# Kernel tuning notes

Measured on AMD Instinct MI355X. Metric: run time of the kernel, lower is better.

The kernel has to match this reference:

```python
import jax, jax.numpy as jnp
import numpy as np

B, C, H, W, NA = 2, 512, 25, 25, 9
A = H * W * NA  # 5625 anchors
PROB_T = 0.5
OVL_T = 0.5


def _make_anchors():
    ys, xs = np.meshgrid(np.arange(H), np.arange(W), indexing='ij')
    cx = (xs + 0.5) / W
    cy = (ys + 0.5) / H
    boxes = []
    for s in (0.1, 0.2, 0.4):
        for r in (0.5, 1.0, 2.0):
            w = s * np.sqrt(r)
            h = s / np.sqrt(r)
            boxes.append(np.stack([cx - w / 2, cy - h / 2, cx + w / 2, cy + h / 2], -1))
    anc = np.stack(boxes, axis=2)  # [H, W, 9, 4] matches [B,H,W,9*4] reshape order
    return jnp.asarray(anc.reshape(-1, 4), jnp.float32)


def setup_inputs() -> dict:
    key = jax.random.key(0)
    ks = jax.random.split(key, 4)
    x = jax.random.normal(ks[0], (B, C, H, W), jnp.float32)
    conv_w = jax.random.normal(ks[1], (512, 512, 3, 3), jnp.float32) * (1.0 / np.sqrt(512 * 9))
    conv_b = jnp.zeros((512,), jnp.float32)
    reg_w = jax.random.normal(ks[2], (36, 512), jnp.float32) * 0.02
    reg_b = jnp.zeros((36,), jnp.float32)
    cls_w = jax.random.normal(ks[3], (9, 512), jnp.float32) * 0.05
    cls_b = jnp.zeros((9,), jnp.float32)
    anchors = _make_anchors()
    return {"x": x, "conv_w": conv_w, "conv_b": conv_b, "reg_w": reg_w,
            "reg_b": reg_b, "cls_w": cls_w, "cls_b": cls_b, "anchors": anchors}


def reference(x, conv_w, conv_b, reg_w, reg_b, cls_w, cls_b, anchors):
    # --- RPN forward ---
    h = jax.lax.conv_general_dilated(x, conv_w, (1, 1), 'SAME',
                                     dimension_numbers=('NCHW', 'OIHW', 'NCHW'))
    h = jax.nn.relu(h + conv_b[None, :, None, None])
    box = jnp.einsum('bchw,oc->bhwo', h, reg_w) + reg_b  # [B,H,W,36] (== permute NHWC)
    cls = jnp.einsum('bchw,oc->bhwo', h, cls_w) + cls_b  # [B,H,W,9]
    offsets = box.reshape(B, A, 4)
    logits = cls.reshape(B, A)
    # --- detect: sigmoid + threshold ---
    probs = jax.nn.sigmoid(logits)
    valid = probs > PROB_T
    # --- box decode: gcxgcy -> cxcy -> xy (SSD-style, anchors given in xy) ---
    a_cx = (anchors[:, 0] + anchors[:, 2]) * 0.5
    a_cy = (anchors[:, 1] + anchors[:, 3]) * 0.5
    a_w = anchors[:, 2] - anchors[:, 0]
    a_h = anchors[:, 3] - anchors[:, 1]
    cx = offsets[..., 0] * a_w / 10.0 + a_cx
    cy = offsets[..., 1] * a_h / 10.0 + a_cy
    bw = jnp.exp(offsets[..., 2] / 5.0) * a_w
    bh = jnp.exp(offsets[..., 3] / 5.0) * a_h
    boxes = jnp.stack([cx - bw / 2, cy - bh / 2, cx + bw / 2, cy + bh / 2], -1)  # [B,A,4]
    # --- sort descending by score; invalid anchors sorted last and pre-suppressed ---
    sort_key = jnp.where(valid, probs, -1.0)
    order = jnp.argsort(-sort_key, axis=-1)
    sb = jnp.take_along_axis(boxes, order[..., None], axis=1)  # sorted boxes
    ss = jnp.take_along_axis(probs, order, axis=1)             # sorted scores
    sv = jnp.take_along_axis(valid, order, axis=1)             # sorted validity

    def per_image(b, v):
        x1, y1, x2, y2 = b[:, 0], b[:, 1], b[:, 2], b[:, 3]
        area = (x2 - x1) * (y2 - y1)
        iw = jnp.clip(jnp.minimum(x2[:, None], x2[None, :]) - jnp.maximum(x1[:, None], x1[None, :]), 0.0)
        ih = jnp.clip(jnp.minimum(y2[:, None], y2[None, :]) - jnp.maximum(y1[:, None], y1[None, :]), 0.0)
        inter = iw * ih
        ov = inter / (area[:, None] + area[None, :] - inter)  # [A,A] Jaccard
        sup0 = (~v).astype(jnp.int32)  # invalid anchors never considered

        def body(i, sup):
            cand = jnp.maximum(sup, (ov[i] > OVL_T).astype(jnp.int32)).at[i].set(0)
            return jnp.where(sup[i] > 0, sup, cand)  # skip if already suppressed

        sup = jax.lax.fori_loop(0, A, body, sup0)
        return (1 - sup) * v.astype(jnp.int32)

    keep = jax.vmap(per_image)(sb, sv)  # [B,A] 1 = kept detection
    return jnp.concatenate([sb, ss[..., None], keep[..., None].astype(jnp.float32)], -1)  # [B,A,6]
```

## Files before the change

### kernel.cpp

```cpp
#include <hip/hip_runtime.h>
#include <cstdint>
#include <cstddef>

#define AA 5625
#define MROWS 5760

__global__ __launch_bounds__(256) void k_wt(const float* __restrict__ cw,
                                            float* __restrict__ wt,
                                            int* __restrict__ Vcnt) {
  if (blockIdx.x == 0 && threadIdx.x < 2) Vcnt[threadIdx.x] = 0;
  __shared__ float t[64][65];
  int kb = (blockIdx.x % 72) * 64;
  int ob = (blockIdx.x / 72) * 64;
  int col = threadIdx.x & 63;
  int rr  = threadIdx.x >> 6;
#pragma unroll
  for (int it = 0; it < 16; ++it) {
    int row = rr + it * 4;
    t[row][col] = cw[(size_t)(ob + row) * 4608 + kb + col];
  }
  __syncthreads();
#pragma unroll
  for (int it = 0; it < 16; ++it) {
    int row = rr + it * 4;
    wt[(size_t)(kb + row) * 512 + ob + col] = t[col][row];
  }
}

__global__ void k_xpad(const float* __restrict__ x, float* __restrict__ xp) {
  int n = blockIdx.x * 256 + threadIdx.x;
  if (n >= 884736) return;
  int c = n & 31;
  int r = (n >> 5) % 27;
  int rest = (n >> 5) / 27;
  float v = 0.f;
  int oy = r - 1, ox = c - 1;
  if (oy >= 0 && oy < 25 && ox >= 0 && ox < 25)
    v = x[(size_t)rest * 625 + oy * 25 + ox];
  xp[n] = v;
}

__global__ __launch_bounds__(256) void k_conv(const float* __restrict__ wt,
                                              const float* __restrict__ xp,
                                              double* __restrict__ hpart,
                                              int Kper) {
  int cpx = gridDim.x >> 3;
  int flat = blockIdx.x;
  int logical = (flat & 7) * cpx + (flat >> 3);
  int sharer = logical % 10;
  int s      = logical / 10;
  int Nt = s & 7;
  int ks = s >> 3;
  int b  = sharer / 5;
  int Mt = sharer % 5;

  int tid = threadIdx.x;
  int m0  = Mt * 128;
  int oc0 = Nt * 64;
  int R  = (tid >> 6) * 32 + ((tid >> 4) & 3) * 8;
  int cb = 2 * (tid & 15);

  __shared__ __align__(16) float As[2][18][128];
  __shared__ __align__(16) float Bs[2][18][64];

  double acc[8][4];
#pragma unroll
  for (int i = 0; i < 8; ++i)
#pragma unroll
    for (int j = 0; j < 4; ++j) acc[i][j] = 0.0;

  int kbase = ks * Kper;
  int nchunk = Kper / 18;

  int ldsoA[9], aoff[9];
#pragma unroll
  for (int t = 0; t < 9; ++t) {
    int s2 = tid + 256 * t;
    int row = s2 >> 7, col = s2 & 127;
    ldsoA[t] = row * 128 + col;
    int m = m0 + col;
    bool av = (m < 625);
    int mm = av ? m : 0;
    int icl = (row >= 9) ? 1 : 0;
    int tap = row - 9 * icl;
    int dy = tap / 3, dx = tap - 3 * dy;
    int yy = mm / 25, xx = mm - yy * 25;
    int ao = (icl * 27 + yy + dy) * 32 + xx + dx;
    aoff[t] = av ? ao : -1;
  }
  int ldsoB[5], boffB[5];
  bool bval[5];
#pragma unroll
  for (int t = 0; t < 5; ++t) {
    int s2 = tid + 256 * t;
    bval[t] = (s2 < 1152);
    int s2c = bval[t] ? s2 : 0;
    int row = s2c >> 6, col = s2c & 63;
    ldsoB[t] = row * 64 + col;
    boffB[t] = row * 512 + oc0 + col;
  }
  const float* wbase = wt + (size_t)kbase * 512;
  const float* abase = xp + (size_t)(b * 512 + kbase / 9) * 864;

  float rA[9], rB[5];

#define LOADCH(CH) {                                                          \
    int k0e = (CH) * (18 * 512);                                              \
    int a0e = (CH) * (2 * 864);                                               \
    _Pragma("unroll")                                                         \
    for (int t = 0; t < 9; ++t)                                               \
      rA[t] = (aoff[t] >= 0) ? abase[a0e + aoff[t]] : 0.f;                    \
    _Pragma("unroll")                                                         \
    for (int t = 0; t < 5; ++t)                                               \
      rB[t] = bval[t] ? wbase[k0e + boffB[t]] : 0.f;                          \
  }
#define WRITECH(BUF) {                                                        \
    _Pragma("unroll")                                                         \
    for (int t = 0; t < 9; ++t)                                               \
      ((float*)As[BUF])[ldsoA[t]] = rA[t];                                    \
    _Pragma("unroll")                                                         \
    for (int t = 0; t < 5; ++t)                                               \
      if (bval[t]) ((float*)Bs[BUF])[ldsoB[t]] = rB[t];                       \
  }

  LOADCH(0);
  WRITECH(0);
  __syncthreads();

  for (int ch = 0; ch < nchunk; ++ch) {
    int cur = ch & 1, nxt = cur ^ 1;
    int chn = (ch + 1 < nchunk) ? (ch + 1) : (nchunk - 1);
    LOADCH(chn);
#pragma unroll 2
    for (int kk = 0; kk < 18; ++kk) {
      float4 a0 = *(const float4*)&As[cur][kk][R];
      float4 a1 = *(const float4*)&As[cur][kk][R + 4];
      float2 b0 = *(const float2*)&Bs[cur][kk][cb];
      float2 b1 = *(const float2*)&Bs[cur][kk][cb + 32];
      double ad[8] = {(double)a0.x, (double)a0.y, (double)a0.z, (double)a0.w,
                      (double)a1.x, (double)a1.y, (double)a1.z, (double)a1.w};
      double bd[4] = {(double)b0.x, (double)b0.y, (double)b1.x, (double)b1.y};
#pragma unroll
      for (int i = 0; i < 8; ++i)
#pragma unroll
        for (int j = 0; j < 4; ++j) acc[i][j] += ad[i] * bd[j];
    }
    if (ch + 1 < nchunk) {
      __syncthreads();
      WRITECH(nxt);
      __syncthreads();
    }
  }

  double* hb = hpart + ((size_t)(ks * 2 + b) * 625) * 512 + oc0 + cb;
#pragma unroll
  for (int i = 0; i < 8; ++i) {
    int mm = m0 + R + i;
    if (mm < 625) {
      double* p = hb + (size_t)mm * 512;
      double2 v0; v0.x = acc[i][0]; v0.y = acc[i][1];
      double2 v1; v1.x = acc[i][2]; v1.y = acc[i][3];
      *(double2*)p        = v0;
      *(double2*)(p + 32) = v1;
    }
  }
#undef LOADCH
#undef WRITECH
}

__device__ __forceinline__ double shfl_down_d(double x, int off) {
  long long v = __double_as_longlong(x);
  int lo = __shfl_down((int)(unsigned int)(v & 0xffffffffLL), off);
  int hi = __shfl_down((int)(v >> 32), off);
  return __longlong_as_double(((long long)hi << 32) | (unsigned int)lo);
}

__global__ __launch_bounds__(256) void k_heads(
    const double* __restrict__ hpart, const float* __restrict__ conv_b,
    const float* __restrict__ reg_w, const float* __restrict__ reg_b,
    const float* __restrict__ cls_w, const float* __restrict__ cls_b,
    const float* __restrict__ anchors, float* __restrict__ boxesraw,
    float* __restrict__ probs, unsigned long long* __restrict__ keys,
    unsigned int* __restrict__ rank, int nsplit) {
  int pos = blockIdx.x % 625;
  int b   = blockIdx.x / 625;
  int tid = threadIdx.x;
  __shared__ double hv[512];
  __shared__ double res[45];
  for (int c = tid; c < 512; c += 256) {
    double s = 0.0;
    for (int k = 0; k < nsplit; ++k)
      s += hpart[(((size_t)k * 2 + b) * 625 + pos) * 512 + c];
    s += (double)conv_b[c];
    hv[c] = s > 0.0 ? s : 0.0;
  }
  __syncthreads();
  int wv = tid >> 6, l = tid & 63;
  for (int o = wv; o < 45; o += 4) {
    const float* wrow = (o < 36) ? (reg_w + (size_t)o * 512)
                                 : (cls_w + (size_t)(o - 36) * 512);
    double s = 0.0;
#pragma unroll
    for (int kk = 0; kk < 8; ++kk)
      s += hv[l + kk * 64] * (double)wrow[l + kk * 64];
#pragma unroll
    for (int d = 32; d > 0; d >>= 1) s += shfl_down_d(s, d);
    if (l == 0) res[o] = s + (double)((o < 36) ? reg_b[o] : cls_b[o - 36]);
  }
  __syncthreads();
  if (tid < 9) {
    int na = tid;
    int a = pos * 9 + na;
    double o0 = res[na * 4 + 0], o1 = res[na * 4 + 1];
    double o2 = res[na * 4 + 2], o3 = res[na * 4 + 3];
    double logit = res[36 + na];
    float4 anc = *(const float4*)(anchors + (size_t)a * 4);
    double a_cx = ((double)anc.x + (double)anc.z) * 0.5;
    double a_cy = ((double)anc.y + (double)anc.w) * 0.5;
    double a_w = (double)anc.z - (double)anc.x;
    double a_h = (double)anc.w - (double)anc.y;
    double cx = o0 * a_w / 10.0 + a_cx;
    double cy = o1 * a_h / 10.0 + a_cy;
    double bw = exp(o2 / 5.0) * a_w;
    double bh = exp(o3 / 5.0) * a_h;
    float4 box = make_float4((float)(cx - bw / 2.0), (float)(cy - bh / 2.0),
                             (float)(cx + bw / 2.0), (float)(cy + bh / 2.0));
    size_t ga = (size_t)b * AA + a;
    *(float4*)(boxesraw + ga * 4) = box;
    float p = (float)(1.0 / (1.0 + exp(-logit)));
    probs[ga] = p;
    bool valid = p > 0.5f;
    float f = -(valid ? p : -1.0f);
    unsigned int u = __float_as_uint(f);
    u = (u & 0x80000000u) ? ~u : (u | 0x80000000u);
    keys[ga] = (((unsigned long long)u) << 32) | (unsigned int)a;
    rank[ga] = 0u;
  }
}

__global__ __launch_bounds__(256) void k_count(
    const unsigned long long* __restrict__ keys, unsigned int* __restrict__ rank) {
  int b = blockIdx.z;
  int i = blockIdx.x * 256 + threadIdx.x;
  __shared__ unsigned long long sj[1024];
  unsigned long long my = (i < AA) ? keys[(size_t)b * AA + i] : 0ULL;
  int j0 = blockIdx.y * 1024;
  for (int jj = threadIdx.x; jj < 1024; jj += 256) {
    int j = j0 + jj;
    sj[jj] = (j < AA) ? keys[(size_t)b * AA + j] : ~0ULL;
  }
  __syncthreads();
  int cnt = 0;
#pragma unroll 8
  for (int jj = 0; jj < 1024; ++jj) cnt += (sj[jj] < my) ? 1 : 0;
  if (i < AA && cnt) atomicAdd(&rank[(size_t)b * AA + i], (unsigned)cnt);
}

__global__ void k_perm(const unsigned long long* __restrict__ keys,
                       const unsigned int* __restrict__ rank,
                       unsigned int* __restrict__ perm, int* __restrict__ Vcnt) {
  int idx = blockIdx.x * 256 + threadIdx.x;
  if (idx >= 2 * AA) return;
  int b = idx / AA, i = idx - b * AA;
  unsigned long long k = keys[idx];
  unsigned int r = rank[idx];
  perm[(size_t)b * AA + r] = (unsigned)i;
  if (!(k >> 63)) atomicAdd(&Vcnt[b], 1);
}

__global__ void k_assembly(const unsigned int* __restrict__ perm,
                           const float* __restrict__ boxesraw,
                           const float* __restrict__ probs,
                           float* __restrict__ out, float4* __restrict__ sb4) {
  int idx = blockIdx.x * 256 + threadIdx.x;
  if (idx >= 2 * AA) return;
  int b = idx / AA;
  unsigned int pa = perm[idx];
  float4 bx = *(const float4*)(boxesraw + ((size_t)b * AA + pa) * 4);
  float p = probs[(size_t)b * AA + pa];
  float* o = out + (size_t)idx * 6;
  o[0] = bx.x; o[1] = bx.y; o[2] = bx.z; o[3] = bx.w; o[4] = p; o[5] = 0.f;
  sb4[idx] = bx;
}

__global__ __launch_bounds__(256) void k_maskT(const float4* __restrict__ sb4,
                                               const int* __restrict__ Vcnt,
                                               ulonglong2* __restrict__ maskT) {
  int b = blockIdx.y;
  int V = Vcnt[b];
  int i = blockIdx.x * 4 + (threadIdx.x >> 6);
  if (i >= V) return;
  int lane = threadIdx.x & 63;
  float4 bif = sb4[(size_t)b * AA + i];
  double bix = bif.x, biy = bif.y, biz = bif.z, biw = bif.w;
  double ai = (biz - bix) * (biw - biy);
  unsigned long long lo = 0, hi = 0;
#pragma unroll 4
  for (int w = 0; w < 88; ++w) {
    int j = w * 64 + lane;
    int jc = (j < AA) ? j : (AA - 1);
    float4 c = sb4[(size_t)b * AA + jc];
    double aj = ((double)c.z - (double)c.x) * ((double)c.w - (double)c.y);
    double iw = fmin(biz, (double)c.z) - fmax(bix, (double)c.x);
    double ih = fmin(biw, (double)c.w) - fmax(biy, (double)c.y);
    iw = iw > 0.0 ? iw : 0.0;
    ih = ih > 0.0 ? ih : 0.0;
    double inter = iw * ih;
    bool bit = (inter + inter > ai + aj - inter) && (j != i) && (j < AA);
    unsigned long long bb = bit ? 1ULL : 0ULL;
    if (w < 64) lo |= bb << w;
    else        hi |= bb << (w - 64);
  }
  ulonglong2 v; v.x = lo; v.y = hi;
  maskT[((size_t)b * MROWS + i) * 64 + lane] = v;
}

#define NMS_STEP(Q, J)                                                        \
  {                                                                           \
    int i = base + (J);                                                       \
    if (i < V) {                                                              \
      int w = i >> 6, t = i & 63;                                             \
      if (t == 0) {                                                           \
        unsigned long long cbit = (w < 64) ? (colLo >> w) : (colHi >> (w - 64)); \
        supw = __ballot((int)(cbit & 1ULL));                                  \
      }                                                                       \
      if (!((supw >> t) & 1ULL)) {                                            \
        colLo |= Q.x; colHi |= Q.y;                                           \
        unsigned long long cbit = (w < 64) ? (colLo >> w) : (colHi >> (w - 64)); \
        supw = __ballot((int)(cbit & 1ULL));                                  \
        if (lane == 0) out[((size_t)b * AA + i) * 6 + 5] = 1.0f;              \
      }                                                                       \
    }                                                                         \
    Q = mt[(size_t)(i + 16) * 64 + lane];                                     \
  }

__global__ __launch_bounds__(64) void k_nms(const ulonglong2* __restrict__ maskT,
                                            const int* __restrict__ Vcnt,
                                            float* __restrict__ out) {
  int b = blockIdx.x;
  int lane = threadIdx.x;
  int V = Vcnt[b];
  const ulonglong2* mt = maskT + (size_t)b * MROWS * 64;
  unsigned long long colLo = 0, colHi = 0, supw = 0;
  ulonglong2 q00 = mt[(size_t)0  * 64 + lane], q01 = mt[(size_t)1  * 64 + lane];
  ulonglong2 q02 = mt[(size_t)2  * 64 + lane], q03 = mt[(size_t)3  * 64 + lane];
  ulonglong2 q04 = mt[(size_t)4  * 64 + lane], q05 = mt[(size_t)5  * 64 + lane];
  ulonglong2 q06 = mt[(size_t)6  * 64 + lane], q07 = mt[(size_t)7  * 64 + lane];
  ulonglong2 q08 = mt[(size_t)8  * 64 + lane], q09 = mt[(size_t)9  * 64 + lane];
  ulonglong2 q10 = mt[(size_t)10 * 64 + lane], q11 = mt[(size_t)11 * 64 + lane];
  ulonglong2 q12 = mt[(size_t)12 * 64 + lane], q13 = mt[(size_t)13 * 64 + lane];
  ulonglong2 q14 = mt[(size_t)14 * 64 + lane], q15 = mt[(size_t)15 * 64 + lane];
  for (int base = 0; base < V; base += 16) {
    NMS_STEP(q00, 0)  NMS_STEP(q01, 1)  NMS_STEP(q02, 2)  NMS_STEP(q03, 3)
    NMS_STEP(q04, 4)  NMS_STEP(q05, 5)  NMS_STEP(q06, 6)  NMS_STEP(q07, 7)
    NMS_STEP(q08, 8)  NMS_STEP(q09, 9)  NMS_STEP(q10, 10) NMS_STEP(q11, 11)
    NMS_STEP(q12, 12) NMS_STEP(q13, 13) NMS_STEP(q14, 14) NMS_STEP(q15, 15)
  }
}
#undef NMS_STEP

extern "C" void kernel_launch(void* const* d_in, const int* in_sizes, int n_in,
                              void* d_out, int out_size, void* d_ws, size_t ws_size,
                              hipStream_t stream) {
  const float* x      = (const float*)d_in[0];
  const float* conv_w = (const float*)d_in[1];
  const float* conv_b = (const float*)d_in[2];
  const float* reg_w  = (const float*)d_in[3];
  const float* reg_b  = (const float*)d_in[4];
  const float* cls_w  = (const float*)d_in[5];
  const float* cls_b  = (const float*)d_in[6];
  const float* anchors= (const float*)d_in[7];
  float* out = (float*)d_out;
  char* ws = (char*)d_ws;

  size_t off = 0;
  auto alloc = [&](size_t bytes) {
    size_t o = off;
    off += (bytes + 255) & ~(size_t)255;
    return o;
  };
  size_t o_wt   = alloc(4608ULL * 512 * 4);
  size_t o_xp   = alloc(884736ULL * 4);
  size_t o_box  = alloc(2ULL * AA * 4 * 4);
  size_t o_prob = alloc(2ULL * AA * 4);
  size_t o_keys = alloc(2ULL * AA * 8);
  size_t o_rank = alloc(2ULL * AA * 4);
  size_t o_perm = alloc(2ULL * AA * 4);
  size_t o_sb4  = alloc(2ULL * AA * 16);
  size_t o_V    = alloc(256);
  size_t o_maskT= alloc(2ULL * MROWS * 64 * 16);
  size_t fixed = off;

  int nsplit = 1;
  const int cands[5] = {16, 8, 4, 2, 1};
  for (int ci = 0; ci < 5; ++ci) {
    size_t need = fixed + (size_t)cands[ci] * 2 * 625 * 512 * 8;
    if (need <= ws_size) { nsplit = cands[ci]; break; }
  }
  size_t o_hp = alloc((size_t)nsplit * 2 * 625 * 512 * 8);

  float* wtp   = (float*)(ws + o_wt);
  float* xpp   = (float*)(ws + o_xp);
  float* boxp  = (float*)(ws + o_box);
  float* probp = (float*)(ws + o_prob);
  unsigned long long* keysp = (unsigned long long*)(ws + o_keys);
  unsigned int* rankp = (unsigned int*)(ws + o_rank);
  unsigned int* permp = (unsigned int*)(ws + o_perm);
  float4* sb4p = (float4*)(ws + o_sb4);
  int* Vp      = (int*)(ws + o_V);
  ulonglong2* maskTp = (ulonglong2*)(ws + o_maskT);
  double* hpp  = (double*)(ws + o_hp);

  k_wt<<<dim3(576), dim3(256), 0, stream>>>(conv_w, wtp, Vp);
  k_xpad<<<dim3(3456), dim3(256), 0, stream>>>(x, xpp);
  k_conv<<<dim3(80 * nsplit), dim3(256), 0, stream>>>(wtp, xpp, hpp, 4608 / nsplit);
  k_heads<<<dim3(1250), dim3(256), 0, stream>>>(hpp, conv_b, reg_w, reg_b,
                                                cls_w, cls_b, anchors, boxp,
                                                probp, keysp, rankp, nsplit);
  k_count<<<dim3(22, 6, 2), dim3(256), 0, stream>>>(keysp, rankp);
  k_perm<<<dim3(44), dim3(256), 0, stream>>>(keysp, rankp, permp, Vp);
  k_assembly<<<dim3(44), dim3(256), 0, stream>>>(permp, boxp, probp, out, sb4p);
  k_maskT<<<dim3(1407, 2), dim3(256), 0, stream>>>(sb4p, Vp, maskTp);
  k_nms<<<dim3(2), dim3(64), 0, stream>>>(maskTp, Vp, out);
}
```

Baseline: 531.6 us.

## Widen conv tile to 128x128 with fp64 LDS staging and unroll split-K reduce

The conv GEMM tile grows from 128x64 to 128x128 output channels per block, so each thread computes an 8x8 fp64 accumulator block. The grid is halved to match. Operands are now converted to double once when written into shared memory, so the inner loop no longer converts each float it reads, and the k-chunk shrinks from 18 to 9 to keep LDS size fixed. The heads kernel also unrolls the split-K partial sum for nsplit=16 so all 16 loads are issued at once. The trade-offs are much higher register pressure (64 fp64 accumulators), fewer blocks, and more LDS bandwidth per element.

After: 698.8 us. 1.31x slower.

```diff
diff --git a/kernel.cpp b/kernel.cpp
--- a/kernel.cpp
+++ b/kernel.cpp
@@ -49,78 +49,71 @@
   int logical = (flat & 7) * cpx + (flat >> 3);
   int sharer = logical % 10;
   int s      = logical / 10;
-  int Nt = s & 7;
-  int ks = s >> 3;
+  int Nt = s & 3;
+  int ks = s >> 2;
   int b  = sharer / 5;
   int Mt = sharer % 5;
 
   int tid = threadIdx.x;
   int m0  = Mt * 128;
-  int oc0 = Nt * 64;
+  int oc0 = Nt * 128;
   int R  = (tid >> 6) * 32 + ((tid >> 4) & 3) * 8;
   int cb = 2 * (tid & 15);
 
-  __shared__ __align__(16) float As[2][18][128];
-  __shared__ __align__(16) float Bs[2][18][64];
-
-  double acc[8][4];
+  __shared__ __align__(16) double As[2][9][128];
+  __shared__ __align__(16) double Bs[2][9][128];
+
+  double acc[8][8];
 #pragma unroll
   for (int i = 0; i < 8; ++i)
 #pragma unroll
-    for (int j = 0; j < 4; ++j) acc[i][j] = 0.0;
+    for (int j = 0; j < 8; ++j) acc[i][j] = 0.0;
 
   int kbase = ks * Kper;
-  int nchunk = Kper / 18;
-
-  int ldsoA[9], aoff[9];
-#pragma unroll
-  for (int t = 0; t < 9; ++t) {
+  int nchunk = Kper / 9;
+
+  int ldso[5], aoff[5], boff[5];
+  bool v4 = (tid < 128);
+#pragma unroll
+  for (int t = 0; t < 5; ++t) {
     int s2 = tid + 256 * t;
+    if (s2 >= 1152) s2 = 0;
     int row = s2 >> 7, col = s2 & 127;
-    ldsoA[t] = row * 128 + col;
+    ldso[t] = row * 128 + col;
+    boff[t] = row * 512 + oc0 + col;
     int m = m0 + col;
     bool av = (m < 625);
     int mm = av ? m : 0;
-    int icl = (row >= 9) ? 1 : 0;
-    int tap = row - 9 * icl;
-    int dy = tap / 3, dx = tap - 3 * dy;
+    int dy = row / 3, dx = row - 3 * dy;
     int yy = mm / 25, xx = mm - yy * 25;
-    int ao = (icl * 27 + yy + dy) * 32 + xx + dx;
-    aoff[t] = av ? ao : -1;
-  }
-  int ldsoB[5], boffB[5];
-  bool bval[5];
-#pragma unroll
-  for (int t = 0; t < 5; ++t) {
-    int s2 = tid + 256 * t;
-    bval[t] = (s2 < 1152);
-    int s2c = bval[t] ? s2 : 0;
-    int row = s2c >> 6, col = s2c & 63;
-    ldsoB[t] = row * 64 + col;
-    boffB[t] = row * 512 + oc0 + col;
+    aoff[t] = av ? ((yy + dy) * 32 + xx + dx) : -1;
   }
   const float* wbase = wt + (size_t)kbase * 512;
   const float* abase = xp + (size_t)(b * 512 + kbase / 9) * 864;
 
-  float rA[9], rB[5];
+  float rA[5], rB[5];
 
 #define LOADCH(CH) {                                                          \
-    int k0e = (CH) * (18 * 512);                                              \
-    int a0e = (CH) * (2 * 864);                                               \
+    int k0e = (CH) * (9 * 512);                                               \
+    int a0e = (CH) * 864;                                                     \
     _Pragma("unroll")                                                         \
-    for (int t = 0; t < 9; ++t)                                               \
+    for (int t = 0; t < 4; ++t) {                                             \
       rA[t] = (aoff[t] >= 0) ? abase[a0e + aoff[t]] : 0.f;                    \
-    _Pragma("unroll")                                                         \
-    for (int t = 0; t < 5; ++t)                                               \
-      rB[t] = bval[t] ? wbase[k0e + boffB[t]] : 0.f;                          \
+      rB[t] = wbase[k0e + boff[t]];                                           \
+    }                                                                         \
+    rA[4] = (v4 && aoff[4] >= 0) ? abase[a0e + aoff[4]] : 0.f;                \
+    rB[4] = v4 ? wbase[k0e + boff[4]] : 0.f;                                  \
   }
 #define WRITECH(BUF) {                                                        \
     _Pragma("unroll")                                                         \
-    for (int t = 0; t < 9; ++t)                                               \
-      ((float*)As[BUF])[ldsoA[t]] = rA[t];                                    \
-    _Pragma("unroll")                                                         \
-    for (int t = 0; t < 5; ++t)                                               \
-      if (bval[t]) ((float*)Bs[BUF])[ldsoB[t]] = rB[t];                       \
+    for (int t = 0; t < 4; ++t) {                                             \
+      ((double*)As[BUF])[ldso[t]] = (double)rA[t];                            \
+      ((double*)Bs[BUF])[ldso[t]] = (double)rB[t];                            \
+    }                                                                         \
+    if (v4) {                                                                 \
+      ((double*)As[BUF])[ldso[4]] = (double)rA[4];                            \
+      ((double*)Bs[BUF])[ldso[4]] = (double)rB[4];                            \
+    }                                                                         \
   }
 
   LOADCH(0);
@@ -131,19 +124,22 @@
     int cur = ch & 1, nxt = cur ^ 1;
     int chn = (ch + 1 < nchunk) ? (ch + 1) : (nchunk - 1);
     LOADCH(chn);
-#pragma unroll 2
-    for (int kk = 0; kk < 18; ++kk) {
-      float4 a0 = *(const float4*)&As[cur][kk][R];
-      float4 a1 = *(const float4*)&As[cur][kk][R + 4];
-      float2 b0 = *(const float2*)&Bs[cur][kk][cb];
-      float2 b1 = *(const float2*)&Bs[cur][kk][cb + 32];
-      double ad[8] = {(double)a0.x, (double)a0.y, (double)a0.z, (double)a0.w,
-                      (double)a1.x, (double)a1.y, (double)a1.z, (double)a1.w};
-      double bd[4] = {(double)b0.x, (double)b0.y, (double)b1.x, (double)b1.y};
+#pragma unroll
+    for (int kk = 0; kk < 9; ++kk) {
+      double2 a0 = *(const double2*)&As[cur][kk][R];
+      double2 a1 = *(const double2*)&As[cur][kk][R + 2];
+      double2 a2 = *(const double2*)&As[cur][kk][R + 4];
+      double2 a3 = *(const double2*)&As[cur][kk][R + 6];
+      double2 b0 = *(const double2*)&Bs[cur][kk][cb];
+      double2 b1 = *(const double2*)&Bs[cur][kk][cb + 32];
+      double2 b2 = *(const double2*)&Bs[cur][kk][cb + 64];
+      double2 b3 = *(const double2*)&Bs[cur][kk][cb + 96];
+      double ad[8] = {a0.x, a0.y, a1.x, a1.y, a2.x, a2.y, a3.x, a3.y};
+      double bd[8] = {b0.x, b0.y, b1.x, b1.y, b2.x, b2.y, b3.x, b3.y};
 #pragma unroll
       for (int i = 0; i < 8; ++i)
 #pragma unroll
-        for (int j = 0; j < 4; ++j) acc[i][j] += ad[i] * bd[j];
+        for (int j = 0; j < 8; ++j) acc[i][j] += ad[i] * bd[j];
     }
     if (ch + 1 < nchunk) {
       __syncthreads();
@@ -158,10 +154,11 @@
     int mm = m0 + R + i;
     if (mm < 625) {
       double* p = hb + (size_t)mm * 512;
-      double2 v0; v0.x = acc[i][0]; v0.y = acc[i][1];
-      double2 v1; v1.x = acc[i][2]; v1.y = acc[i][3];
-      *(double2*)p        = v0;
-      *(double2*)(p + 32) = v1;
+#pragma unroll
+      for (int r = 0; r < 4; ++r) {
+        double2 v; v.x = acc[i][2 * r]; v.y = acc[i][2 * r + 1];
+        *(double2*)(p + 32 * r) = v;
+      }
     }
   }
 #undef LOADCH
@@ -187,10 +184,24 @@
   int tid = threadIdx.x;
   __shared__ double hv[512];
   __shared__ double res[45];
+  const size_t kstr = (size_t)2 * 625 * 512;
   for (int c = tid; c < 512; c += 256) {
-    double s = 0.0;
-    for (int k = 0; k < nsplit; ++k)
-      s += hpart[(((size_t)k * 2 + b) * 625 + pos) * 512 + c];
+    const double* hp = hpart + ((size_t)b * 625 + pos) * 512 + c;
+    double s;
+    if (nsplit == 16) {
+      double t0 = hp[0],          t1 = hp[kstr],      t2 = hp[2 * kstr],
+             t3 = hp[3 * kstr],   t4 = hp[4 * kstr],  t5 = hp[5 * kstr],
+             t6 = hp[6 * kstr],   t7 = hp[7 * kstr],  t8 = hp[8 * kstr],
+             t9 = hp[9 * kstr],   t10 = hp[10 * kstr], t11 = hp[11 * kstr],
+             t12 = hp[12 * kstr], t13 = hp[13 * kstr], t14 = hp[14 * kstr],
+             t15 = hp[15 * kstr];
+      s = t0; s += t1; s += t2; s += t3; s += t4; s += t5; s += t6; s += t7;
+      s += t8; s += t9; s += t10; s += t11; s += t12; s += t13; s += t14;
+      s += t15;
+    } else {
+      s = 0.0;
+      for (int k = 0; k < nsplit; ++k) s += hp[(size_t)k * kstr];
+    }
     s += (double)conv_b[c];
     hv[c] = s > 0.0 ? s : 0.0;
   }
@@ -413,7 +424,7 @@
 
   k_wt<<<dim3(576), dim3(256), 0, stream>>>(conv_w, wtp, Vp);
   k_xpad<<<dim3(3456), dim3(256), 0, stream>>>(x, xpp);
-  k_conv<<<dim3(80 * nsplit), dim3(256), 0, stream>>>(wtp, xpp, hpp, 4608 / nsplit);
+  k_conv<<<dim3(40 * nsplit), dim3(256), 0, stream>>>(wtp, xpp, hpp, 4608 / nsplit);
   k_heads<<<dim3(1250), dim3(256), 0, stream>>>(hpp, conv_b, reg_w, reg_b,
                                                 cls_w, cls_b, anchors, boxp,
                                                 probp, keysp, rankp, nsplit);
```
